# Performance work log

Hardware: AMD Instinct MI355X
Metric: run time of the kernel (lower is better)

The kernel has to match this reference:

```python
import jax, jax.numpy as jnp
import numpy as np

EPS = 1e-07

def _ciou(preds, targets, eps=EPS):
    # xywh -> corner boxes
    x1, y1, w1, h1 = preds[:, 0], preds[:, 1], preds[:, 2], preds[:, 3]
    x2, y2, w2, h2 = targets[:, 0], targets[:, 1], targets[:, 2], targets[:, 3]
    w1_, h1_, w2_, h2_ = w1 / 2, h1 / 2, w2 / 2, h2 / 2
    b1x1, b1x2, b1y1, b1y2 = x1 - w1_, x1 + w1_, y1 - h1_, y1 + h1_
    b2x1, b2x2, b2y1, b2y2 = x2 - w2_, x2 + w2_, y2 - h2_, y2 + h2_
    # intersection
    iw = jnp.clip(jnp.minimum(b1x2, b2x2) - jnp.maximum(b1x1, b2x1), 0)
    ih = jnp.clip(jnp.minimum(b1y2, b2y2) - jnp.maximum(b1y1, b2y1), 0)
    inter = iw * ih
    union = w1 * h1 + w2 * h2 - inter + eps
    iou = inter / union
    # enclosing box
    cw = jnp.maximum(b1x2, b2x2) - jnp.minimum(b1x1, b2x1)
    ch = jnp.maximum(b1y2, b2y2) - jnp.minimum(b1y1, b2y1)
    c2 = cw * cw + ch * ch + eps  # squared diagonal of enclosing box
    # squared center distance
    rho2 = ((b2x1 + b2x2 - b1x1 - b1x2) ** 2 + (b2y1 + b2y2 - b1y1 - b1y2) ** 2) / 4
    # aspect-ratio consistency term
    v = (4 / np.pi ** 2) * (jnp.arctan(w2 / (h2 + eps)) - jnp.arctan(w1 / (h1 + eps))) ** 2
    alpha = jax.lax.stop_gradient(v / (v - iou + (1 + eps)))  # torch.no_grad in original
    return iou - (rho2 / c2 + v * alpha)


def setup_inputs() -> dict:
    key = jax.random.key(0)
    k1, k2 = jax.random.split(key)
    M = 4_000_000
    preds = jax.random.uniform(k1, (M, 4), dtype=jnp.float32)
    targets = jax.random.uniform(k2, (M, 4), dtype=jnp.float32)
    return {"preds": preds, "targets": targets}


def reference(preds, targets):
    num_targets = targets.shape[0]
    ciou = _ciou(preds, targets)
    # original: sum over per-box (1 - ciou) divided by number of targets
    return jnp.sum(1.0 - ciou) / num_targets
```

## Files before the change

kernel.cpp:

```cpp
#include <hip/hip_runtime.h>
#include <math.h>

#define EPS 1e-7f
#define NBLOCKS 2048
#define NTHREADS 256
#define UNROLL 8

__device__ __forceinline__ float fast_rcp(float x) {
    return __builtin_amdgcn_rcpf(x);
}

__device__ __forceinline__ float fast_atan(float q) {
    float aq  = fabsf(q);
    float inv = fast_rcp(aq);
    float t   = fminf(aq, inv);
    float t2  = t * t;
    float p = -0.0117212f;
    p = fmaf(p, t2,  0.05265332f);
    p = fmaf(p, t2, -0.11643287f);
    p = fmaf(p, t2,  0.19354346f);
    p = fmaf(p, t2, -0.33262347f);
    p = fmaf(p, t2,  0.99997726f);
    p = p * t;
    float r = (aq > 1.0f) ? (1.57079632679f - p) : p;
    return copysignf(r, q);
}

__device__ __forceinline__ float ciou_loss_elem(float4 p, float4 t) {
    float x1 = p.x, y1 = p.y, w1 = p.z, h1 = p.w;
    float x2 = t.x, y2 = t.y, w2 = t.z, h2 = t.w;

    float w1h = 0.5f * w1, h1h = 0.5f * h1;
    float w2h = 0.5f * w2, h2h = 0.5f * h2;

    float b1x1 = x1 - w1h, b1x2 = x1 + w1h;
    float b1y1 = y1 - h1h, b1y2 = y1 + h1h;
    float b2x1 = x2 - w2h, b2x2 = x2 + w2h;
    float b2y1 = y2 - h2h, b2y2 = y2 + h2h;

    float iw = fmaxf(fminf(b1x2, b2x2) - fmaxf(b1x1, b2x1), 0.0f);
    float ih = fmaxf(fminf(b1y2, b2y2) - fmaxf(b1y1, b2y1), 0.0f);
    float inter = iw * ih;
    float uni = w1 * h1 + w2 * h2 - inter + EPS;
    float iou = inter * fast_rcp(uni);

    float cw = fmaxf(b1x2, b2x2) - fminf(b1x1, b2x1);
    float ch = fmaxf(b1y2, b2y2) - fminf(b1y1, b2y1);
    float c2 = cw * cw + ch * ch + EPS;

    float dx = x2 - x1, dy = y2 - y1;
    float rho2 = fmaf(dx, dx, dy * dy);

    float h1e = h1 + EPS, h2e = h2 + EPS;
    float num = w2 * h1e - w1 * h2e;
    float den = fmaf(h1e, h2e, w1 * w2);
    float da  = fast_atan(num * fast_rcp(den));

    const float c4pi2 = 4.0f / (float)(M_PI * M_PI);
    float v = c4pi2 * da * da;
    float alpha = v * fast_rcp(v - iou + (1.0f + EPS));

    return 1.0f - iou + rho2 * fast_rcp(c2) + v * alpha;
}

__global__ __launch_bounds__(NTHREADS) void ciou_partial_kernel(
    const float4* __restrict__ preds,
    const float4* __restrict__ targets,
    float* __restrict__ partials,
    int m)
{
    int tid = blockIdx.x * NTHREADS + threadIdx.x;
    const int S = NBLOCKS * NTHREADS;

    float4 p[UNROLL], t[UNROLL];
    int idx[UNROLL];
    #pragma unroll
    for (int u = 0; u < UNROLL; ++u) {
        idx[u] = tid + u * S;
        int j = (idx[u] < m) ? idx[u] : 0;
        p[u] = preds[j];
        t[u] = targets[j];
    }

    float acc = 0.0f;
    #pragma unroll
    for (int u = 0; u < UNROLL; ++u) {
        float val = ciou_loss_elem(p[u], t[u]);
        acc += (idx[u] < m) ? val : 0.0f;
    }

    #pragma unroll
    for (int off = 32; off > 0; off >>= 1)
        acc += __shfl_down(acc, off, 64);

    __shared__ float wsum[4];
    int lane = threadIdx.x & 63;
    int wid  = threadIdx.x >> 6;
    if (lane == 0) wsum[wid] = acc;
    __syncthreads();
    if (threadIdx.x == 0)
        partials[blockIdx.x] = wsum[0] + wsum[1] + wsum[2] + wsum[3];
}

__global__ __launch_bounds__(NTHREADS) void ciou_final_kernel(
    const float* __restrict__ partials,
    int nblocks,
    float* __restrict__ out,
    float inv_m)
{
    double acc = 0.0;
    for (int i = threadIdx.x; i < nblocks; i += NTHREADS)
        acc += (double)partials[i];

    #pragma unroll
    for (int off = 32; off > 0; off >>= 1)
        acc += __shfl_down(acc, off, 64);

    __shared__ double wsum[4];
    int lane = threadIdx.x & 63;
    int wid  = threadIdx.x >> 6;
    if (lane == 0) wsum[wid] = acc;
    __syncthreads();
    if (threadIdx.x == 0)
        out[0] = (float)((wsum[0] + wsum[1] + wsum[2] + wsum[3]) * (double)inv_m);
}

extern "C" void kernel_launch(void* const* d_in, const int* in_sizes, int n_in,
                              void* d_out, int out_size, void* d_ws, size_t ws_size,
                              hipStream_t stream)
{
    const float4* preds   = (const float4*)d_in[0];
    const float4* targets = (const float4*)d_in[1];
    float* out = (float*)d_out;
    float* partials = (float*)d_ws;

    int m = in_sizes[0] / 4;

    ciou_partial_kernel<<<NBLOCKS, NTHREADS, 0, stream>>>(preds, targets, partials, m);
    ciou_final_kernel<<<1, NTHREADS, 0, stream>>>(partials, NBLOCKS, out, 1.0f / (float)m);
}
```

Baseline: 29.62 us.

## Use contiguous per-block chunks with larger unroll and fewer blocks

Halves the grid to 1024 blocks and doubles per-thread work to 16 boxes. Each block now covers one contiguous chunk instead of grid-strided slices, and loads are interleaved with compute in a single loop. It also drops the sign restoration in atan, since only the square is used, and builds the corner coordinates with FMAs. The change depends on the compiler still hoisting loads for memory-level parallelism, and fewer blocks could underfill the GPU. Coverage is exactly 1024*256*16 = 4,194,304 elements, so any input larger than that would be silently truncated.

Result: faster. 26.48 us (median of 2 runs) (-10.6%).

```diff
diff --git a/kernel.cpp b/kernel.cpp
--- a/kernel.cpp
+++ b/kernel.cpp
@@ -2,15 +2,15 @@
 #include <math.h>
 
 #define EPS 1e-7f
-#define NBLOCKS 2048
+#define NBLOCKS 1024
 #define NTHREADS 256
-#define UNROLL 8
+#define UNROLL 16
 
 __device__ __forceinline__ float fast_rcp(float x) {
     return __builtin_amdgcn_rcpf(x);
 }
 
-__device__ __forceinline__ float fast_atan(float q) {
+__device__ __forceinline__ float fast_atan_sq_arg(float q) {
     float aq  = fabsf(q);
     float inv = fast_rcp(aq);
     float t   = fminf(aq, inv);
@@ -22,21 +22,17 @@
     p = fmaf(p, t2, -0.33262347f);
     p = fmaf(p, t2,  0.99997726f);
     p = p * t;
-    float r = (aq > 1.0f) ? (1.57079632679f - p) : p;
-    return copysignf(r, q);
+    return (aq > 1.0f) ? (1.57079632679f - p) : p;
 }
 
 __device__ __forceinline__ float ciou_loss_elem(float4 p, float4 t) {
     float x1 = p.x, y1 = p.y, w1 = p.z, h1 = p.w;
     float x2 = t.x, y2 = t.y, w2 = t.z, h2 = t.w;
 
-    float w1h = 0.5f * w1, h1h = 0.5f * h1;
-    float w2h = 0.5f * w2, h2h = 0.5f * h2;
-
-    float b1x1 = x1 - w1h, b1x2 = x1 + w1h;
-    float b1y1 = y1 - h1h, b1y2 = y1 + h1h;
-    float b2x1 = x2 - w2h, b2x2 = x2 + w2h;
-    float b2y1 = y2 - h2h, b2y2 = y2 + h2h;
+    float b1x1 = fmaf(-0.5f, w1, x1), b1x2 = fmaf(0.5f, w1, x1);
+    float b1y1 = fmaf(-0.5f, h1, y1), b1y2 = fmaf(0.5f, h1, y1);
+    float b2x1 = fmaf(-0.5f, w2, x2), b2x2 = fmaf(0.5f, w2, x2);
+    float b2y1 = fmaf(-0.5f, h2, y2), b2y2 = fmaf(0.5f, h2, y2);
 
     float iw = fmaxf(fminf(b1x2, b2x2) - fmaxf(b1x1, b2x1), 0.0f);
     float ih = fmaxf(fminf(b1y2, b2y2) - fmaxf(b1y1, b2y1), 0.0f);
@@ -54,7 +50,7 @@
     float h1e = h1 + EPS, h2e = h2 + EPS;
     float num = w2 * h1e - w1 * h2e;
     float den = fmaf(h1e, h2e, w1 * w2);
-    float da  = fast_atan(num * fast_rcp(den));
+    float da  = fast_atan_sq_arg(num * fast_rcp(den));
 
     const float c4pi2 = 4.0f / (float)(M_PI * M_PI);
     float v = c4pi2 * da * da;
@@ -69,24 +65,19 @@
     float* __restrict__ partials,
     int m)
 {
-    int tid = blockIdx.x * NTHREADS + threadIdx.x;
-    const int S = NBLOCKS * NTHREADS;
-
-    float4 p[UNROLL], t[UNROLL];
-    int idx[UNROLL];
-    #pragma unroll
-    for (int u = 0; u < UNROLL; ++u) {
-        idx[u] = tid + u * S;
-        int j = (idx[u] < m) ? idx[u] : 0;
-        p[u] = preds[j];
-        t[u] = targets[j];
-    }
+    const int base = blockIdx.x * (NTHREADS * UNROLL) + threadIdx.x;
 
     float acc = 0.0f;
-    #pragma unroll
-    for (int u = 0; u < UNROLL; ++u) {
-        float val = ciou_loss_elem(p[u], t[u]);
-        acc += (idx[u] < m) ? val : 0.0f;
+    if (base < m) {
+        #pragma unroll
+        for (int u = 0; u < UNROLL; ++u) {
+            int idx = base + u * NTHREADS;
+            int j = (idx < m) ? idx : 0;
+            float4 p = preds[j];
+            float4 t = targets[j];
+            float val = ciou_loss_elem(p, t);
+            acc += (idx < m) ? val : 0.0f;
+        }
     }
 
     #pragma unroll
```
